# Optimization experiments

Hardware: AMD Instinct MI355X
Metric: run time of the kernel (lower is better)

## Reference

```python
import jax, jax.numpy as jnp
import numpy as np

L, N, E, H = 2048, 2, 1024, 16
D = E // H  # head dim = 64


def setup_inputs() -> dict:
    key = jax.random.key(0)
    k1, k2, k3, k4, k5 = jax.random.split(key, 5)
    s = 1.0 / np.sqrt(E)
    return {
        "x": jax.random.normal(k1, (L, N, E), dtype=jnp.float32),
        "in_proj_weight": jax.random.normal(k2, (3 * E, E), dtype=jnp.float32) * s,
        "in_proj_bias": jax.random.normal(k3, (3 * E,), dtype=jnp.float32) * 0.01,
        "out_proj_weight": jax.random.normal(k4, (E, E), dtype=jnp.float32) * s,
        "out_proj_bias": jax.random.normal(k5, (E,), dtype=jnp.float32) * 0.01,
    }


def reference(x, in_proj_weight, in_proj_bias, out_proj_weight, out_proj_bias):
    # packed qkv in-projection: (L, N, 3E)
    qkv = jnp.einsum("lne,fe->lnf", x, in_proj_weight) + in_proj_bias
    q, k, v = jnp.split(qkv, 3, axis=-1)

    def heads(t):  # (L, N, E) -> (N, H, L, D)
        return t.reshape(L, N, H, D).transpose(1, 2, 0, 3)

    q, k, v = heads(q), heads(k), heads(v)
    scale = 1.0 / jnp.sqrt(jnp.asarray(D, dtype=q.dtype))
    scores = jnp.einsum("nhld,nhmd->nhlm", q * scale, k)  # (N, H, L, L)
    attn = jax.nn.softmax(scores, axis=-1)
    out = jnp.einsum("nhlm,nhmd->nhld", attn, v)  # (N, H, L, D)
    out = out.transpose(2, 0, 1, 3).reshape(L, N, E)
    return jnp.einsum("lne,fe->lnf", out, out_proj_weight) + out_proj_bias
```

## Files before the change

### kernel.cpp

```cpp
#include <hip/hip_runtime.h>

typedef __attribute__((ext_vector_type(8))) short bf16x8;
typedef __attribute__((ext_vector_type(4))) float f32x4;
typedef __attribute__((ext_vector_type(16))) float f32x16;
typedef __attribute__((ext_vector_type(8))) unsigned short ushort8;
typedef __attribute__((ext_vector_type(4))) unsigned short ushort4_t;
typedef __attribute__((ext_vector_type(4))) unsigned uint4_t;

#define LSEQ 2048
#define NB 2
#define EMB 1024
#define NHEAD 16
#define HD 64

__device__ __forceinline__ unsigned short f2bf(float f) {
  unsigned u = __builtin_bit_cast(unsigned, f);
  u += 0x7fffu + ((u >> 16) & 1u);
  return (unsigned short)(u >> 16);
}
__device__ __forceinline__ float bf2f(unsigned short s) {
  return __builtin_bit_cast(float, ((unsigned)s) << 16);
}

__device__ __forceinline__ void gll16(const void* g, void* l) {
  __builtin_amdgcn_global_load_lds((const __attribute__((address_space(1))) unsigned*)g,
                                   (__attribute__((address_space(3))) unsigned*)l, 16, 0, 0);
}

__global__ __launch_bounds__(256) void cvt_all(const float* __restrict__ x,
                                               const float* __restrict__ wq,
                                               const float* __restrict__ wo,
                                               unsigned short* __restrict__ xb,
                                               unsigned short* __restrict__ wqb,
                                               unsigned short* __restrict__ wob) {
  int i = blockIdx.x * 256 + threadIdx.x;
  const float* src;
  unsigned short* dst;
  int off;
  if (i < 1048576) { src = x;  dst = xb;  off = i; }
  else if (i < 1835008) { src = wq; dst = wqb; off = i - 1048576; }
  else { src = wo; dst = wob; off = i - 1835008; }
  float4 v = ((const float4*)src)[off];
  ushort4_t o;
  o.x = f2bf(v.x); o.y = f2bf(v.y); o.z = f2bf(v.z); o.w = f2bf(v.w);
  ((ushort4_t*)dst)[off] = o;
}

template <bool OUT_BF16>
__global__ __launch_bounds__(256, 3) void gemm_bf16_nt(
    const unsigned short* __restrict__ A, const unsigned short* __restrict__ B,
    const float* __restrict__ bias, void* __restrict__ Cout, int M, int Ncol, int K) {
  __shared__ unsigned short Asm[128 * 64];
  __shared__ unsigned short Bsm[128 * 64];
  const int tid = threadIdx.x;
  const int wave = tid >> 6, lane = tid & 63;
  const int wr = (wave >> 1) * 64, wc = (wave & 1) * 64;
  const int lr = lane & 15, lg = lane >> 4;
  const int bm = blockIdx.x * 128, bn = blockIdx.y * 128;

  f32x4 acc[4][4];
#pragma unroll
  for (int i = 0; i < 4; ++i)
#pragma unroll
    for (int j = 0; j < 4; ++j) acc[i][j] = (f32x4){0.f, 0.f, 0.f, 0.f};

  for (int kt = 0; kt < K; kt += 64) {
#pragma unroll
    for (int c = 0; c < 4; ++c) {
      int idx = (c * 4 + wave) * 64 + lane;
      int row = idx >> 3, ch = (idx & 7) * 8;
      gll16(A + (size_t)(bm + row) * K + kt + ch, &Asm[(c * 4 + wave) * 512]);
      gll16(B + (size_t)(bn + row) * K + kt + ch, &Bsm[(c * 4 + wave) * 512]);
    }
    __syncthreads();
#pragma unroll
    for (int ks = 0; ks < 2; ++ks) {
      bf16x8 af[4], bfr[4];
#pragma unroll
      for (int i = 0; i < 4; ++i)
        af[i] = *(const bf16x8*)&Asm[(wr + i * 16 + lr) * 64 + ks * 32 + lg * 8];
#pragma unroll
      for (int j = 0; j < 4; ++j)
        bfr[j] = *(const bf16x8*)&Bsm[(wc + j * 16 + lr) * 64 + ks * 32 + lg * 8];
      __builtin_amdgcn_s_setprio(1);
#pragma unroll
      for (int i = 0; i < 4; ++i)
#pragma unroll
        for (int j = 0; j < 4; ++j)
          acc[i][j] = __builtin_amdgcn_mfma_f32_16x16x32_bf16(af[i], bfr[j], acc[i][j], 0, 0, 0);
      __builtin_amdgcn_s_setprio(0);
    }
    __syncthreads();
  }
#pragma unroll
  for (int i = 0; i < 4; ++i) {
#pragma unroll
    for (int j = 0; j < 4; ++j) {
      int col = bn + wc + j * 16 + lr;
      float bv = bias[col];
#pragma unroll
      for (int r = 0; r < 4; ++r) {
        int row = bm + wr + i * 16 + lg * 4 + r;
        float v = acc[i][j][r] + bv;
        if constexpr (OUT_BF16)
          ((unsigned short*)Cout)[(size_t)row * Ncol + col] = f2bf(v);
        else
          ((float*)Cout)[(size_t)row * Ncol + col] = v;
      }
    }
  }
}

__global__ __launch_bounds__(256) void transpose_v(const unsigned short* __restrict__ qkv,
                                                   unsigned short* __restrict__ vt) {
  __shared__ unsigned short t[64][72];
  const int nh = blockIdx.y, n = nh >> 4, h = nh & 15;
  const int lt = blockIdx.x * 64;
  const int tid = threadIdx.x;
#pragma unroll
  for (int it = 0; it < 2; ++it) {
    int idx = it * 256 + tid;
    int l = idx >> 3, ch = (idx & 7) * 8;
    ushort8 v = *(const ushort8*)(qkv + (size_t)((lt + l) * NB + n) * 3072 + 2 * EMB + h * HD + ch);
    *(ushort8*)&t[l][ch] = v;
  }
  __syncthreads();
  int d = tid >> 2, lc = (tid & 3) * 16;
  unsigned short tmp[16];
#pragma unroll
  for (int i = 0; i < 16; ++i) tmp[i] = t[lc + i][d];
#pragma unroll
  for (int i = 0; i < 2; ++i)
    *(ushort8*)(vt + (size_t)(nh * HD + d) * LSEQ + lt + lc + i * 8) = *(const ushort8*)&tmp[i * 8];
}

__global__ __launch_bounds__(256, 4) void flash_attn(const unsigned short* __restrict__ qkv,
                                                     const unsigned short* __restrict__ vt,
                                                     float* __restrict__ Op,
                                                     float* __restrict__ Lp) {
  __shared__ unsigned short Ksm[2][64 * 64];
  __shared__ unsigned short Vsm[2][64 * 64];
  const int tid = threadIdx.x, wave = tid >> 6, lane = tid & 63;
  const int l31 = lane & 31, lh = lane >> 5;
  const int flat = blockIdx.x;
  const int fb = (flat & 7) * 128 + (flat >> 3);
  const int nh = fb >> 5, rem = fb & 31;
  const int qt = rem >> 1, half = rem & 1;
  const int n = nh >> 4, hh = nh & 15;
  const int q = qt * 128 + wave * 32 + l31;
  const int key0 = half * (LSEQ / 2);

  const int sch = ((lane & 7) ^ ((lane >> 3) & 7)) * 8;
  const unsigned short* Kbase = qkv + (size_t)n * 3072 + EMB + hh * HD + sch;
  const unsigned short* Vbase = vt + (size_t)nh * HD * LSEQ + sch;

  bf16x8 qf[4];
  {
    const unsigned short* qb = qkv + ((size_t)q * NB + n) * 3072 + hh * HD + lh * 8;
#pragma unroll
    for (int t = 0; t < 4; ++t) {
      bf16x8 tv = *(const bf16x8*)(qb + t * 16);
#pragma unroll
      for (int e = 0; e < 8; ++e)
        tv[e] = (short)f2bf(bf2f((unsigned short)tv[e]) * 0.18033688f);
      qf[t] = tv;
    }
  }

  auto stage = [&](int buf, int kt) {
#pragma unroll
    for (int c = 0; c < 2; ++c) {
      int row = ((c * 4 + wave) * 64 + lane) >> 3;
      gll16(Kbase + (size_t)(key0 + kt * 64 + row) * (NB * 3072), &Ksm[buf][(c * 4 + wave) * 512]);
      gll16(Vbase + (size_t)row * LSEQ + key0 + kt * 64, &Vsm[buf][(c * 4 + wave) * 512]);
    }
  };

  float lsum = 0.f;
  f32x16 o0, o1, zv;
#pragma unroll
  for (int r = 0; r < 16; ++r) { o0[r] = 0.f; o1[r] = 0.f; zv[r] = 0.f; }

  stage(0, 0);
  __syncthreads();
  int cur = 0;
  const int swz = l31 & 7;
  const int NT = (LSEQ / 2) / 64;

  for (int kt = 0; kt < NT; ++kt) {
    if (kt < NT - 1) stage(cur ^ 1, kt + 1);

    f32x16 s0, s1;
    __builtin_amdgcn_s_setprio(1);
    {
      int ch = (lh ^ swz) * 8;
      bf16x8 k0 = *(const bf16x8*)&Ksm[cur][l31 * 64 + ch];
      bf16x8 k1 = *(const bf16x8*)&Ksm[cur][(32 + l31) * 64 + ch];
      s0 = __builtin_amdgcn_mfma_f32_32x32x16_bf16(k0, qf[0], zv, 0, 0, 0);
      s1 = __builtin_amdgcn_mfma_f32_32x32x16_bf16(k1, qf[0], zv, 0, 0, 0);
    }
#pragma unroll
    for (int t = 1; t < 4; ++t) {
      int ch = ((t * 2 + lh) ^ swz) * 8;
      bf16x8 k0 = *(const bf16x8*)&Ksm[cur][l31 * 64 + ch];
      bf16x8 k1 = *(const bf16x8*)&Ksm[cur][(32 + l31) * 64 + ch];
      s0 = __builtin_amdgcn_mfma_f32_32x32x16_bf16(k0, qf[t], s0, 0, 0, 0);
      s1 = __builtin_amdgcn_mfma_f32_32x32x16_bf16(k1, qf[t], s1, 0, 0, 0);
    }
    __builtin_amdgcn_s_setprio(0);

    float ps0 = 0.f, ps1 = 0.f, ps2 = 0.f, ps3 = 0.f;
#pragma unroll
    for (int r = 0; r < 16; r += 4) {
      float a0 = exp2f(s0[r]),     b0 = exp2f(s1[r]);
      float a1 = exp2f(s0[r + 1]), b1 = exp2f(s1[r + 1]);
      float a2 = exp2f(s0[r + 2]), b2 = exp2f(s1[r + 2]);
      float a3 = exp2f(s0[r + 3]), b3 = exp2f(s1[r + 3]);
      s0[r] = a0; s0[r + 1] = a1; s0[r + 2] = a2; s0[r + 3] = a3;
      s1[r] = b0; s1[r + 1] = b1; s1[r + 2] = b2; s1[r + 3] = b3;
      ps0 += a0 + b0; ps1 += a1 + b1; ps2 += a2 + b2; ps3 += a3 + b3;
    }
    lsum += (ps0 + ps1) + (ps2 + ps3);

    bf16x8 pf[4];
#pragma unroll
    for (int g = 0; g < 4; ++g) {
      const int b = (g & 1) * 8;
      float a0 = (g < 2) ? s0[b + 0] : s1[b + 0];
      float a1 = (g < 2) ? s0[b + 1] : s1[b + 1];
      float a2 = (g < 2) ? s0[b + 2] : s1[b + 2];
      float a3 = (g < 2) ? s0[b + 3] : s1[b + 3];
      float a4 = (g < 2) ? s0[b + 4] : s1[b + 4];
      float a5 = (g < 2) ? s0[b + 5] : s1[b + 5];
      float a6 = (g < 2) ? s0[b + 6] : s1[b + 6];
      float a7 = (g < 2) ? s0[b + 7] : s1[b + 7];
      unsigned w0, w1, w2, w3;
      asm("v_cvt_pk_bf16_f32 %0, %1, %2" : "=v"(w0) : "v"(a0), "v"(a1));
      asm("v_cvt_pk_bf16_f32 %0, %1, %2" : "=v"(w1) : "v"(a2), "v"(a3));
      asm("v_cvt_pk_bf16_f32 %0, %1, %2" : "=v"(w2) : "v"(a4), "v"(a5));
      asm("v_cvt_pk_bf16_f32 %0, %1, %2" : "=v"(w3) : "v"(a6), "v"(a7));
      asm("v_permlane32_swap_b32 %0, %1" : "+v"(w0), "+v"(w2));
      asm("v_permlane32_swap_b32 %0, %1" : "+v"(w1), "+v"(w3));
      pf[g] = __builtin_bit_cast(bf16x8, (uint4_t){w0, w1, w2, w3});
    }

    __builtin_amdgcn_s_setprio(1);
#pragma unroll
    for (int u = 0; u < 4; ++u) {
      int ch = ((u * 2 + lh) ^ swz) * 8;
      bf16x8 a0 = *(const bf16x8*)&Vsm[cur][l31 * 64 + ch];
      bf16x8 a1 = *(const bf16x8*)&Vsm[cur][(32 + l31) * 64 + ch];
      o0 = __builtin_amdgcn_mfma_f32_32x32x16_bf16(a0, pf[u], o0, 0, 0, 0);
      o1 = __builtin_amdgcn_mfma_f32_32x32x16_bf16(a1, pf[u], o1, 0, 0, 0);
    }
    __builtin_amdgcn_s_setprio(0);

    __syncthreads();
    cur ^= 1;
  }

  float* op = Op + (size_t)half * (4096 * 1024) + ((size_t)q * NB + n) * EMB + hh * HD;
#pragma unroll
  for (int g = 0; g < 4; ++g) {
    float4 pk0, pk1;
    pk0.x = o0[g * 4 + 0]; pk0.y = o0[g * 4 + 1]; pk0.z = o0[g * 4 + 2]; pk0.w = o0[g * 4 + 3];
    pk1.x = o1[g * 4 + 0]; pk1.y = o1[g * 4 + 1]; pk1.z = o1[g * 4 + 2]; pk1.w = o1[g * 4 + 3];
    *(float4*)(op + g * 8 + lh * 4) = pk0;
    *(float4*)(op + 32 + g * 8 + lh * 4) = pk1;
  }
  lsum += __shfl_xor(lsum, 32);
  if (lh == 0)
    Lp[(size_t)half * 65536 + ((size_t)q * NB + n) * NHEAD + hh] = lsum;
}

__global__ __launch_bounds__(256) void combine_o(const float* __restrict__ Op,
                                                 const float* __restrict__ Lp,
                                                 unsigned short* __restrict__ ob) {
  int i = blockIdx.x * 256 + threadIdx.x;
  float4 a = ((const float4*)Op)[i];
  float4 b = ((const float4*)(Op + 4096 * 1024))[i];
  int e = i << 2;
  int qn = e >> 10, h = (e >> 6) & 15;
  float l = Lp[qn * NHEAD + h] + Lp[65536 + qn * NHEAD + h];
  float inv = 1.0f / l;
  ushort4_t o;
  o.x = f2bf((a.x + b.x) * inv);
  o.y = f2bf((a.y + b.y) * inv);
  o.z = f2bf((a.z + b.z) * inv);
  o.w = f2bf((a.w + b.w) * inv);
  ((ushort4_t*)ob)[i] = o;
}

extern "C" void kernel_launch(void* const* d_in, const int* in_sizes, int n_in,
                              void* d_out, int out_size, void* d_ws, size_t ws_size,
                              hipStream_t stream) {
  const float* x = (const float*)d_in[0];
  const float* wqkv = (const float*)d_in[1];
  const float* bqkv = (const float*)d_in[2];
  const float* wout = (const float*)d_in[3];
  const float* bout = (const float*)d_in[4];

  char* ws = (char*)d_ws;
  unsigned short* xb    = (unsigned short*)(ws);
  unsigned short* wqkvb = (unsigned short*)(ws + 8388608);
  unsigned short* woutb = (unsigned short*)(ws + 14680064);
  unsigned short* qkvb  = (unsigned short*)(ws + 16777216);
  unsigned short* vtb   = (unsigned short*)(ws + 41943040);
  unsigned short* obuf  = (unsigned short*)(ws + 50331648);
  float*          Op    = (float*)(ws + 58720256);
  float*          Lp    = (float*)(ws + 92274688);

  cvt_all<<<8192, 256, 0, stream>>>(x, wqkv, wout, xb, wqkvb, woutb);

  dim3 g1(32, 24);
  gemm_bf16_nt<true><<<g1, 256, 0, stream>>>(xb, wqkvb, bqkv, qkvb, 4096, 3072, 1024);

  dim3 gt(32, 32);
  transpose_v<<<gt, 256, 0, stream>>>(qkvb, vtb);

  flash_attn<<<1024, 256, 0, stream>>>(qkvb, vtb, Op, Lp);
  combine_o<<<4096, 256, 0, stream>>>(Op, Lp, obuf);

  dim3 g3(32, 8);
  gemm_bf16_nt<false><<<g3, 256, 0, stream>>>(obuf, woutb, bout, d_out, 4096, 1024, 1024);
}
```

Baseline: 210.4 us.

## Template GEMM tile sizes and overlap flash-attn K/V prefetch with partial waits

The GEMM is templated on its block tile shape, and the output projection now uses 128x64 tiles, which doubles its grid from 256 to 512 blocks so more CUs have work. In the flash attention loop, the blanket __syncthreads after staging is replaced by an explicit s_waitcnt vmcnt(4) plus s_barrier. Only the current buffer's loads are waited on while the next tile's prefetch stays in flight. The partial wait relies on the exact count of outstanding loads per stage, so it is fragile if the load count or the compiler's instruction order changes.

Measured after the change: 206.0 us. 2.1% less time.

```diff
diff --git a/kernel.cpp b/kernel.cpp
--- a/kernel.cpp
+++ b/kernel.cpp
@@ -46,56 +46,63 @@
   ((ushort4_t*)dst)[off] = o;
 }
 
-template <bool OUT_BF16>
+template <int BM, int BN, bool OUT_BF16>
 __global__ __launch_bounds__(256, 3) void gemm_bf16_nt(
     const unsigned short* __restrict__ A, const unsigned short* __restrict__ B,
     const float* __restrict__ bias, void* __restrict__ Cout, int M, int Ncol, int K) {
-  __shared__ unsigned short Asm[128 * 64];
-  __shared__ unsigned short Bsm[128 * 64];
+  constexpr int MF = BM / 32;
+  constexpr int NF = BN / 32;
+  __shared__ unsigned short Asm[BM * 64];
+  __shared__ unsigned short Bsm[BN * 64];
   const int tid = threadIdx.x;
   const int wave = tid >> 6, lane = tid & 63;
-  const int wr = (wave >> 1) * 64, wc = (wave & 1) * 64;
+  const int wr = (wave >> 1) * (BM / 2), wc = (wave & 1) * (BN / 2);
   const int lr = lane & 15, lg = lane >> 4;
-  const int bm = blockIdx.x * 128, bn = blockIdx.y * 128;
-
-  f32x4 acc[4][4];
-#pragma unroll
-  for (int i = 0; i < 4; ++i)
-#pragma unroll
-    for (int j = 0; j < 4; ++j) acc[i][j] = (f32x4){0.f, 0.f, 0.f, 0.f};
+  const int bm = blockIdx.x * BM, bn = blockIdx.y * BN;
+
+  f32x4 acc[MF][NF];
+#pragma unroll
+  for (int i = 0; i < MF; ++i)
+#pragma unroll
+    for (int j = 0; j < NF; ++j) acc[i][j] = (f32x4){0.f, 0.f, 0.f, 0.f};
 
   for (int kt = 0; kt < K; kt += 64) {
 #pragma unroll
-    for (int c = 0; c < 4; ++c) {
-      int idx = (c * 4 + wave) * 64 + lane;
-      int row = idx >> 3, ch = (idx & 7) * 8;
-      gll16(A + (size_t)(bm + row) * K + kt + ch, &Asm[(c * 4 + wave) * 512]);
-      gll16(B + (size_t)(bn + row) * K + kt + ch, &Bsm[(c * 4 + wave) * 512]);
+    for (int c = 0; c < BM / 32; ++c) {
+      int cc = c * 4 + wave;
+      int row = cc * 8 + (lane >> 3), ch = (lane & 7) * 8;
+      gll16(A + (size_t)(bm + row) * K + kt + ch, &Asm[cc * 512]);
+    }
+#pragma unroll
+    for (int c = 0; c < BN / 32; ++c) {
+      int cc = c * 4 + wave;
+      int row = cc * 8 + (lane >> 3), ch = (lane & 7) * 8;
+      gll16(B + (size_t)(bn + row) * K + kt + ch, &Bsm[cc * 512]);
     }
     __syncthreads();
 #pragma unroll
     for (int ks = 0; ks < 2; ++ks) {
-      bf16x8 af[4], bfr[4];
-#pragma unroll
-      for (int i = 0; i < 4; ++i)
+      bf16x8 af[MF], bfr[NF];
+#pragma unroll
+      for (int i = 0; i < MF; ++i)
         af[i] = *(const bf16x8*)&Asm[(wr + i * 16 + lr) * 64 + ks * 32 + lg * 8];
 #pragma unroll
-      for (int j = 0; j < 4; ++j)
+      for (int j = 0; j < NF; ++j)
         bfr[j] = *(const bf16x8*)&Bsm[(wc + j * 16 + lr) * 64 + ks * 32 + lg * 8];
       __builtin_amdgcn_s_setprio(1);
 #pragma unroll
-      for (int i = 0; i < 4; ++i)
-#pragma unroll
-        for (int j = 0; j < 4; ++j)
+      for (int i = 0; i < MF; ++i)
+#pragma unroll
+        for (int j = 0; j < NF; ++j)
           acc[i][j] = __builtin_amdgcn_mfma_f32_16x16x32_bf16(af[i], bfr[j], acc[i][j], 0, 0, 0);
       __builtin_amdgcn_s_setprio(0);
     }
     __syncthreads();
   }
 #pragma unroll
-  for (int i = 0; i < 4; ++i) {
-#pragma unroll
-    for (int j = 0; j < 4; ++j) {
+  for (int i = 0; i < MF; ++i) {
+#pragma unroll
+    for (int j = 0; j < NF; ++j) {
       int col = bn + wc + j * 16 + lr;
       float bv = bias[col];
 #pragma unroll
@@ -182,13 +189,17 @@
   for (int r = 0; r < 16; ++r) { o0[r] = 0.f; o1[r] = 0.f; zv[r] = 0.f; }
 
   stage(0, 0);
-  __syncthreads();
   int cur = 0;
   const int swz = l31 & 7;
   const int NT = (LSEQ / 2) / 64;
 
   for (int kt = 0; kt < NT; ++kt) {
     if (kt < NT - 1) stage(cur ^ 1, kt + 1);
+    __builtin_amdgcn_sched_barrier(0);
+    if (kt < NT - 1) asm volatile("s_waitcnt vmcnt(4)" ::: "memory");
+    else             asm volatile("s_waitcnt vmcnt(0)" ::: "memory");
+    __builtin_amdgcn_s_barrier();
+    __builtin_amdgcn_sched_barrier(0);
 
     f32x16 s0, s1;
     __builtin_amdgcn_s_setprio(1);
@@ -255,7 +266,8 @@
     }
     __builtin_amdgcn_s_setprio(0);
 
-    __syncthreads();
+    __builtin_amdgcn_sched_barrier(0);
+    __builtin_amdgcn_s_barrier();
     cur ^= 1;
   }
 
@@ -313,7 +325,7 @@
   cvt_all<<<8192, 256, 0, stream>>>(x, wqkv, wout, xb, wqkvb, woutb);
 
   dim3 g1(32, 24);
-  gemm_bf16_nt<true><<<g1, 256, 0, stream>>>(xb, wqkvb, bqkv, qkvb, 4096, 3072, 1024);
+  gemm_bf16_nt<128, 128, true><<<g1, 256, 0, stream>>>(xb, wqkvb, bqkv, qkvb, 4096, 3072, 1024);
 
   dim3 gt(32, 32);
   transpose_v<<<gt, 256, 0, stream>>>(qkvb, vtb);
@@ -321,6 +333,6 @@
   flash_attn<<<1024, 256, 0, stream>>>(qkvb, vtb, Op, Lp);
   combine_o<<<4096, 256, 0, stream>>>(Op, Lp, obuf);
 
-  dim3 g3(32, 8);
-  gemm_bf16_nt<false><<<g3, 256, 0, stream>>>(obuf, woutb, bout, d_out, 4096, 1024, 1024);
-}
+  dim3 g3(32, 16);
+  gemm_bf16_nt<128, 64, false><<<g3, 256, 0, stream>>>(obuf, woutb, bout, d_out, 4096, 1024, 1024);
+}
```
